# Kernel tuning notes

Measured on AMD Instinct MI355X. Metric: run time of the kernel, lower is better.

The kernel has to match this reference:

```python
import jax, jax.numpy as jnp
import numpy as np

VALUE_CONST = 0.5
ENTROPIE_CONST = 0.005


def setup_inputs() -> dict:
    key = jax.random.key(0)
    k1, k2, k3, k4, k5 = jax.random.split(key, 5)
    B, L, V = 16, 512, 32000
    return {
        "pred": jax.random.uniform(k1, (B, L, V), dtype=jnp.float32, minval=1e-6, maxval=1.0),
        "action_probs": jax.random.uniform(k2, (B, L), dtype=jnp.float32, minval=1e-6, maxval=1.0),
        "value": jax.random.normal(k3, (B, L), dtype=jnp.float32),
        "critic_value": jax.random.normal(k4, (B, L), dtype=jnp.float32),
        "segments": jax.random.randint(k5, (B, L), 0, 2, dtype=jnp.int32),
    }


def _segment_logprob(action_probs, segments):
    # Every position in a segment (segment = run ending at a nonzero marker,
    # marker position inclusive) gets that segment's total log-prob sum.
    B, L = action_probs.shape
    logp = jnp.log(action_probs)
    seg = segments.astype(jnp.int32)
    seg_id = jnp.cumsum(seg, axis=1) - seg                      # [B,L] exclusive cumsum
    gid = (jnp.arange(B, dtype=jnp.int32)[:, None] * (L + 1) + seg_id).reshape(-1)
    sums = jax.ops.segment_sum(logp.reshape(-1), gid, num_segments=B * (L + 1))
    segment_prob = jnp.take_along_axis(sums.reshape(B, L + 1), seg_id, axis=1)  # [B,L]
    # Faithful to the original loop: the trailing tail (positions after the last
    # marker) of the LAST batch row is never written and stays zero.
    n_seg = jnp.sum(seg, axis=1)                                 # markers per row
    tail_of_last_row = (seg_id == n_seg[:, None]) & (jnp.arange(B)[:, None] == B - 1)
    return jnp.where(tail_of_last_row, jnp.float32(0.0), segment_prob)


def reference(pred, action_probs, value, critic_value, segments):
    advantage = value - critic_value                             # [B,L]
    log_sum_action_probs = _segment_logprob(action_probs, segments)
    policy_loss = -jnp.mean(jax.lax.stop_gradient(advantage) * log_sum_action_probs)
    value_loss = jnp.mean(advantage * advantage)
    entropy = -jnp.sum(pred * jnp.log(pred), axis=-1)            # [B,L]
    entropy_loss = -jnp.mean(entropy)
    return policy_loss + VALUE_CONST * value_loss + ENTROPIE_CONST * entropy_loss
```

## Files before the change

### kernel.cpp

```cpp
#include <hip/hip_runtime.h>
#include <hip/hip_bf16.h>


#define B_DIM 16
#define L_DIM 512
#define V_DIM 32000

__global__ __launch_bounds__(256) void entropy_sum_kernel(
    const float4* __restrict__ pred4, long long n4, double* __restrict__ ws) {
    long long idx    = (long long)blockIdx.x * blockDim.x + threadIdx.x;
    long long stride = (long long)gridDim.x * blockDim.x;

    double acc = 0.0;
    for (long long i = idx; i < n4; i += stride) {
        float4 p = pred4[i];
        float s = p.x * __logf(p.x) + p.y * __logf(p.y) +
                  p.z * __logf(p.z) + p.w * __logf(p.w);
        acc += (double)s;
    }

    for (int off = 32; off > 0; off >>= 1)
        acc += __shfl_down(acc, off, 64);

    __shared__ double s_wave[4];
    int lane = threadIdx.x & 63;
    int wave = threadIdx.x >> 6;
    if (lane == 0) s_wave[wave] = acc;
    __syncthreads();
    if (threadIdx.x == 0) {
        double blk = s_wave[0] + s_wave[1] + s_wave[2] + s_wave[3];
        atomicAdd(ws, blk);
    }
}

__global__ __launch_bounds__(64) void small_and_combine_kernel(
    const float* __restrict__ action_probs,
    const float* __restrict__ value,
    const float* __restrict__ critic_value,
    const int*   __restrict__ segments,
    const double* __restrict__ ws,
    float* __restrict__ out) {
    __shared__ double s_pol[B_DIM];
    __shared__ double s_adv2[B_DIM];

    int b = threadIdx.x;
    if (b < B_DIM) {
        const float* ap = action_probs + (long long)b * L_DIM;
        const float* va = value        + (long long)b * L_DIM;
        const float* cv = critic_value + (long long)b * L_DIM;
        const int*   sg = segments     + (long long)b * L_DIM;

        double pol = 0.0, adv2 = 0.0;
        float run_logp = 0.0f;
        float run_adv  = 0.0f;
        for (int l = 0; l < L_DIM; ++l) {
            float lp  = __logf(ap[l]);
            float adv = va[l] - cv[l];
            run_logp += lp;
            run_adv  += adv;
            adv2     += (double)adv * (double)adv;
            if (sg[l] != 0) {
                pol += (double)run_logp * (double)run_adv;
                run_logp = 0.0f;
                run_adv  = 0.0f;
            }
        }
        if (b != B_DIM - 1)
            pol += (double)run_logp * (double)run_adv;

        s_pol[b]  = pol;
        s_adv2[b] = adv2;
    }
    __syncthreads();

    if (threadIdx.x == 0) {
        double P = 0.0, A2 = 0.0;
        for (int i = 0; i < B_DIM; ++i) { P += s_pol[i]; A2 += s_adv2[i]; }
        double S = ws[0];
        double res = (-P + 0.5 * A2 + 0.005 * S) / (double)(B_DIM * L_DIM);
        out[0] = (float)res;
    }
}

extern "C" void kernel_launch(void* const* d_in, const int* in_sizes, int n_in,
                              void* d_out, int out_size, void* d_ws, size_t ws_size,
                              hipStream_t stream) {
    const float* pred         = (const float*)d_in[0];
    const float* action_probs = (const float*)d_in[1];
    const float* value        = (const float*)d_in[2];
    const float* critic_value = (const float*)d_in[3];
    const int*   segments     = (const int*)d_in[4];
    float* out = (float*)d_out;
    double* ws = (double*)d_ws;

    hipMemsetAsync(ws, 0, sizeof(double), stream);

    long long n4 = (long long)B_DIM * L_DIM * V_DIM / 4;
    entropy_sum_kernel<<<2048, 256, 0, stream>>>((const float4*)pred, n4, ws);
    small_and_combine_kernel<<<1, 64, 0, stream>>>(action_probs, value,
                                                   critic_value, segments,
                                                   ws, out);
}
```

Measured before the change: 1.323 ms.

## Replace atomic accumulation with per-block partials and stage small loss inputs in LDS

Result: faster. 1.282 ms (-3.0%).

```diff
diff --git a/kernel.cpp b/kernel.cpp
--- a/kernel.cpp
+++ b/kernel.cpp
@@ -5,15 +5,20 @@
 #define B_DIM 16
 #define L_DIM 512
 #define V_DIM 32000
+#define NBLK  2048
+#define TPB   256
 
-__global__ __launch_bounds__(256) void entropy_sum_kernel(
-    const float4* __restrict__ pred4, long long n4, double* __restrict__ ws) {
-    long long idx    = (long long)blockIdx.x * blockDim.x + threadIdx.x;
-    long long stride = (long long)gridDim.x * blockDim.x;
+typedef float vfloat4 __attribute__((ext_vector_type(4)));
+
+__global__ __launch_bounds__(TPB) void entropy_sum_kernel(
+    const vfloat4* __restrict__ pred4, double* __restrict__ partials) {
+    long long idx    = (long long)blockIdx.x * TPB + threadIdx.x;
+    const long long stride = (long long)NBLK * TPB;
+    const long long n4 = (long long)B_DIM * L_DIM * V_DIM / 4;
 
     double acc = 0.0;
     for (long long i = idx; i < n4; i += stride) {
-        float4 p = pred4[i];
+        vfloat4 p = __builtin_nontemporal_load(&pred4[i]);
         float s = p.x * __logf(p.x) + p.y * __logf(p.y) +
                   p.z * __logf(p.z) + p.w * __logf(p.w);
         acc += (double)s;
@@ -22,61 +27,75 @@
     for (int off = 32; off > 0; off >>= 1)
         acc += __shfl_down(acc, off, 64);
 
-    __shared__ double s_wave[4];
-    int lane = threadIdx.x & 63;
-    int wave = threadIdx.x >> 6;
-    if (lane == 0) s_wave[wave] = acc;
+    __shared__ double s_wave[TPB / 64];
+    if ((threadIdx.x & 63) == 0) s_wave[threadIdx.x >> 6] = acc;
     __syncthreads();
-    if (threadIdx.x == 0) {
-        double blk = s_wave[0] + s_wave[1] + s_wave[2] + s_wave[3];
-        atomicAdd(ws, blk);
-    }
+    if (threadIdx.x == 0)
+        partials[blockIdx.x] = s_wave[0] + s_wave[1] + s_wave[2] + s_wave[3];
 }
 
-__global__ __launch_bounds__(64) void small_and_combine_kernel(
+__global__ __launch_bounds__(512) void finish_kernel(
     const float* __restrict__ action_probs,
     const float* __restrict__ value,
     const float* __restrict__ critic_value,
     const int*   __restrict__ segments,
-    const double* __restrict__ ws,
+    const double* __restrict__ partials,
     float* __restrict__ out) {
-    __shared__ double s_pol[B_DIM];
-    __shared__ double s_adv2[B_DIM];
+    __shared__ float         lpL[8][L_DIM];
+    __shared__ float         adL[8][L_DIM];
+    __shared__ unsigned char sgL[8][L_DIM];
+    __shared__ double rowPol[B_DIM];
+    __shared__ double rowA2[B_DIM];
+    __shared__ double sred[512 / 64];
 
-    int b = threadIdx.x;
-    if (b < B_DIM) {
-        const float* ap = action_probs + (long long)b * L_DIM;
-        const float* va = value        + (long long)b * L_DIM;
-        const float* cv = critic_value + (long long)b * L_DIM;
-        const int*   sg = segments     + (long long)b * L_DIM;
+    double s = 0.0;
+    for (int k = 0; k < NBLK / 512; ++k)
+        s += partials[threadIdx.x + 512 * k];
+    for (int off = 32; off > 0; off >>= 1)
+        s += __shfl_down(s, off, 64);
+    if ((threadIdx.x & 63) == 0) sred[threadIdx.x >> 6] = s;
 
-        double pol = 0.0, adv2 = 0.0;
-        float run_logp = 0.0f;
-        float run_adv  = 0.0f;
-        for (int l = 0; l < L_DIM; ++l) {
-            float lp  = __logf(ap[l]);
-            float adv = va[l] - cv[l];
-            run_logp += lp;
-            run_adv  += adv;
-            adv2     += (double)adv * (double)adv;
-            if (sg[l] != 0) {
-                pol += (double)run_logp * (double)run_adv;
-                run_logp = 0.0f;
-                run_adv  = 0.0f;
+    for (int phase = 0; phase < 2; ++phase) {
+        const int rbase = phase * 8;
+        for (int k = 0; k < 8; ++k) {
+            int idx = threadIdx.x + 512 * k;
+            int r = idx >> 9, l = idx & 511;
+            long long g = (long long)(rbase + r) * L_DIM + l;
+            lpL[r][l] = __logf(action_probs[g]);
+            adL[r][l] = value[g] - critic_value[g];
+            sgL[r][l] = (unsigned char)(segments[g] != 0);
+        }
+        __syncthreads();
+        if (threadIdx.x < 8) {
+            int r = threadIdx.x;
+            int row = rbase + r;
+            double pol = 0.0, a2 = 0.0;
+            float run_lp = 0.0f, run_ad = 0.0f;
+            for (int l = 0; l < L_DIM; ++l) {
+                float lp  = lpL[r][l];
+                float adv = adL[r][l];
+                run_lp += lp;
+                run_ad += adv;
+                a2 += (double)adv * (double)adv;
+                if (sgL[r][l]) {
+                    pol += (double)run_lp * (double)run_ad;
+                    run_lp = 0.0f;
+                    run_ad = 0.0f;
+                }
             }
+            if (row != B_DIM - 1)
+                pol += (double)run_lp * (double)run_ad;
+            rowPol[row] = pol;
+            rowA2[row]  = a2;
         }
-        if (b != B_DIM - 1)
-            pol += (double)run_logp * (double)run_adv;
-
-        s_pol[b]  = pol;
-        s_adv2[b] = adv2;
+        __syncthreads();
     }
-    __syncthreads();
 
     if (threadIdx.x == 0) {
         double P = 0.0, A2 = 0.0;
-        for (int i = 0; i < B_DIM; ++i) { P += s_pol[i]; A2 += s_adv2[i]; }
-        double S = ws[0];
+        for (int i = 0; i < B_DIM; ++i) { P += rowPol[i]; A2 += rowA2[i]; }
+        double S = 0.0;
+        for (int i = 0; i < 512 / 64; ++i) S += sred[i];
         double res = (-P + 0.5 * A2 + 0.005 * S) / (double)(B_DIM * L_DIM);
         out[0] = (float)res;
     }
@@ -91,13 +110,9 @@
     const float* critic_value = (const float*)d_in[3];
     const int*   segments     = (const int*)d_in[4];
     float* out = (float*)d_out;
-    double* ws = (double*)d_ws;
+    double* partials = (double*)d_ws;
 
-    hipMemsetAsync(ws, 0, sizeof(double), stream);
-
-    long long n4 = (long long)B_DIM * L_DIM * V_DIM / 4;
-    entropy_sum_kernel<<<2048, 256, 0, stream>>>((const float4*)pred, n4, ws);
-    small_and_combine_kernel<<<1, 64, 0, stream>>>(action_probs, value,
-                                                   critic_value, segments,
-                                                   ws, out);
+    entropy_sum_kernel<<<NBLK, TPB, 0, stream>>>((const vfloat4*)pred, partials);
+    finish_kernel<<<1, 512, 0, stream>>>(action_probs, value, critic_value,
+                                         segments, partials, out);
 }
```
